# Kernel optimization log

Measured on AMD Instinct MI355X. Metric: run time of the kernel, lower is better.

Reference implementation:

```python
import jax, jax.numpy as jnp
import numpy as np

B, N, M, D = 8, 512, 64, 128
H = 64  # mlp_hidden_dim


def setup_inputs() -> dict:
    key = jax.random.key(0)
    ks = jax.random.split(key, 10)
    op_emb = jax.random.normal(ks[0], (B, N, D), dtype=jnp.float32)
    machine_emb = jax.random.normal(ks[1], (B, M, D), dtype=jnp.float32)
    edge_emb = jax.random.normal(ks[2], (B, N, M, D), dtype=jnp.float32)
    action_mask = jax.random.randint(ks[3], (B, N, M), 0, 2) > 0
    s1 = 1.0 / np.sqrt(3 * D)
    s2 = 1.0 / np.sqrt(H)
    W1 = jax.random.uniform(ks[4], (3 * D, H), jnp.float32, -s1, s1)
    b1 = jax.random.uniform(ks[5], (H,), jnp.float32, -s1, s1)
    W2 = jax.random.uniform(ks[6], (H, H), jnp.float32, -s2, s2)
    b2 = jax.random.uniform(ks[7], (H,), jnp.float32, -s2, s2)
    W3 = jax.random.uniform(ks[8], (H, 1), jnp.float32, -s2, s2)
    b3 = jax.random.uniform(ks[9], (1,), jnp.float32, -s2, s2)
    return {"op_emb": op_emb, "machine_emb": machine_emb, "edge_emb": edge_emb,
            "action_mask": action_mask,
            "W1": W1, "b1": b1, "W2": W2, "b2": b2, "W3": W3, "b3": b3}


def reference(op_emb, machine_emb, edge_emb, action_mask, W1, b1, W2, b2, W3, b3):
    # Split first linear over the three concat chunks to avoid materializing
    # the (B,N,M,3D) concat tensor (same math as cat -> Linear).
    Wo, Wm, We = W1[:D], W1[D:2 * D], W1[2 * D:]
    h = (jnp.einsum('bnd,dh->bnh', op_emb, Wo)[:, :, None, :]
         + jnp.einsum('bmd,dh->bmh', machine_emb, Wm)[:, None, :, :]
         + jnp.einsum('bnmd,dh->bnmh', edge_emb, We) + b1)  # (B,N,M,H)
    h = jax.nn.relu(h)
    h = jax.nn.relu(h @ W2 + b2)
    scores = (h @ W3 + b3)[..., 0]  # (B,N,M)
    scores = jnp.where(action_mask, scores, -jnp.inf)
    return jax.nn.log_softmax(scores.reshape(B, N * M), axis=-1)
```

## Files before the change

### kernel.cpp

```cpp
#include <hip/hip_runtime.h>
#include <math.h>

#define Bb 8
#define Nn 512
#define Mm 64
#define Dd 128
#define Hh 64
#define Gg 8
#define NEG_BIG (-1.0e30f)

#define SEGF 260
#define BUFF (8 * SEGF)

typedef __bf16 bf16x8 __attribute__((ext_vector_type(8)));
typedef float  f32x4  __attribute__((ext_vector_type(4)));

#define WS_WEB   0u
#define WS_W2B   16384u
#define WS_CWSF  24576u
#define WS_AOP   155648u
#define WS_SCORE 1204224u
#define WS_PART  2252800u

#define GLOAD_LDS(gp, lp) __builtin_amdgcn_global_load_lds( \
    (const __attribute__((address_space(1))) void*)(gp),    \
    (__attribute__((address_space(3))) void*)(lp), 16, 0, 0)

__global__ __launch_bounds__(256) void prep_kernel(
    const float* __restrict__ W1, const float* __restrict__ W2,
    const float* __restrict__ op_emb, const float* __restrict__ machine_emb,
    const float* __restrict__ b1, char* __restrict__ ws)
{
    if (blockIdx.x < 48) {
        __bf16* WeB = (__bf16*)(ws + WS_WEB);
        __bf16* W2B = (__bf16*)(ws + WS_W2B);
        int idx = blockIdx.x * 256 + threadIdx.x;
        if (idx < 8192) {
            int fid = idx >> 9, rem = idx & 511;
            int lane = rem >> 3, j = rem & 7;
            int t = fid >> 2, ks = fid & 3;
            int q = lane >> 4, ln = lane & 15;
            int d = ks * 32 + q * 8 + j;
            int h = t * 16 + ln;
            WeB[idx] = (__bf16)W1[(size_t)(2 * Dd + d) * Hh + h];
        } else {
            int i2 = idx - 8192;
            int fid = i2 >> 9, rem = i2 & 511;
            int lane = rem >> 3, j = rem & 7;
            int t = fid >> 1, ks = fid & 1;
            int q = lane >> 4, ln = lane & 15;
            int k = ks * 32 + q * 8 + j;
            int h = t * 16 + ln;
            W2B[i2] = (__bf16)W2[(size_t)k * Hh + h];
        }
        return;
    }
    float* CwsF = (float*)(ws + WS_CWSF);
    float* Aop  = (float*)(ws + WS_AOP);
    const int bid = (blockIdx.x - 48) * 4 + (threadIdx.x >> 6);
    const int h = threadIdx.x & 63;
    if (bid < Bb * Mm) {
        const float* mg = machine_emb + (size_t)bid * Dd;
        const float* Wm = W1 + (size_t)Dd * Hh;
        float acc = b1[h];
#pragma unroll 8
        for (int d = 0; d < Dd; ++d) acc = fmaf(mg[d], Wm[d * Hh + h], acc);
        int b = bid >> 6, m = bid & 63;
        int wq = m >> 4, q = (m >> 2) & 3, r = m & 3;
        int t = h >> 4, ln = h & 15;
        CwsF[((((b * 4 + wq) * 4 + t) * 64) + (q * 16 + ln)) * 4 + r] = acc;
    } else {
        const int bn = bid - Bb * Mm;
        const float* og = op_emb + (size_t)bn * Dd;
        float acc = 0.f;
#pragma unroll 8
        for (int d = 0; d < Dd; ++d) acc = fmaf(og[d], W1[d * Hh + h], acc);
        Aop[(size_t)bn * Hh + h] = acc;
    }
}

__global__ __launch_bounds__(256, 2) void main_kernel(
    const float* __restrict__ edge_emb, const int* __restrict__ mask,
    const float* __restrict__ b2, const float* __restrict__ W3,
    const float* __restrict__ b3, char* __restrict__ ws)
{
    __shared__ float  sEdge[4 * 2 * BUFF];
    __shared__ float  sAop[Gg * Hh];
    __shared__ int    sMask[Gg * Mm];
    __shared__ __bf16 sH1[Mm * 72];
    __shared__ float  sRed[8];

    float* scores = (float*)(ws + WS_SCORE);
    float* part   = (float*)(ws + WS_PART);

    const int tid  = threadIdx.x;
    const int lane = tid & 63;
    const int w    = tid >> 6;
    const int q    = lane >> 4;
    const int ln   = lane & 15;
    const int bn0  = blockIdx.x * Gg;
    const int b    = bn0 >> 9;
    const int wu   = __builtin_amdgcn_readfirstlane(w);

    const float* ebase = edge_emb + (size_t)bn0 * (Mm * Dd) + w * 2048 + lane * 4;

    {
        float* d0 = &sEdge[(wu * 2 + 0) * BUFF];
        float* d1 = &sEdge[(wu * 2 + 1) * BUFF];
#pragma unroll
        for (int s = 0; s < 8; ++s) GLOAD_LDS(ebase + s * 256, d0 + s * SEGF);
#pragma unroll
        for (int s = 0; s < 8; ++s) GLOAD_LDS(ebase + 8192 + s * 256, d1 + s * SEGF);
    }

    if (tid < 128) {
        ((f32x4*)sAop)[tid] = ((const f32x4*)(ws + WS_AOP))[(size_t)bn0 * 16 + tid];
        ((int4*)sMask)[tid] = ((const int4*)mask)[(size_t)bn0 * 16 + tid];
    }

    bf16x8 weF[16], w2F[8];
    f32x4  cv[4];
    {
        const bf16x8* WeB = (const bf16x8*)(ws + WS_WEB);
        const bf16x8* W2B = (const bf16x8*)(ws + WS_W2B);
#pragma unroll
        for (int f = 0; f < 16; ++f) weF[f] = WeB[f * 64 + lane];
#pragma unroll
        for (int f = 0; f < 8; ++f)  w2F[f] = W2B[f * 64 + lane];
        const f32x4* CwsF = (const f32x4*)(ws + WS_CWSF) + (size_t)b * 1024;
#pragma unroll
        for (int t = 0; t < 4; ++t)  cv[t] = CwsF[(w * 4 + t) * 64 + lane];
    }

    float b2v[4], w3v[4];
#pragma unroll
    for (int t = 0; t < 4; ++t) { b2v[t] = b2[t * 16 + ln]; w3v[t] = W3[t * 16 + ln]; }
    const float bias3 = b3[0];

    const int rdoff = (ln >> 1) * SEGF + (ln & 1) * 128 + q * 8;

    float m_loc = NEG_BIG, l_loc = 0.f;

    __syncthreads();

#pragma unroll
    for (int g = 0; g < Gg; ++g) {
        const int buf = g & 1;
        const float* ldsrd = &sEdge[(wu * 2 + buf) * BUFF];

        if (g == Gg - 1) __builtin_amdgcn_s_waitcnt(0x0F70);
        else             __builtin_amdgcn_s_waitcnt(0x0F78);

        f32x4 lo[4], hi[4];
#pragma unroll
        for (int ks = 0; ks < 4; ++ks) {
            lo[ks] = *(const f32x4*)&ldsrd[rdoff + ks * 32];
            hi[ks] = *(const f32x4*)&ldsrd[rdoff + ks * 32 + 4];
        }
        bf16x8 af[4];
#pragma unroll
        for (int ks = 0; ks < 4; ++ks) {
            bf16x8 a;
            a[0] = (__bf16)lo[ks][0]; a[1] = (__bf16)lo[ks][1];
            a[2] = (__bf16)lo[ks][2]; a[3] = (__bf16)lo[ks][3];
            a[4] = (__bf16)hi[ks][0]; a[5] = (__bf16)hi[ks][1];
            a[6] = (__bf16)hi[ks][2]; a[7] = (__bf16)hi[ks][3];
            af[ks] = a;
        }

        if (g + 2 < Gg) {
            float* dst = &sEdge[(wu * 2 + buf) * BUFF];
            const float* src = ebase + (size_t)(g + 2) * 8192;
#pragma unroll
            for (int s = 0; s < 8; ++s) GLOAD_LDS(src + s * 256, dst + s * SEGF);
        }

        f32x4 acc[4];
#pragma unroll
        for (int t = 0; t < 4; ++t) {
            float av = sAop[g * Hh + t * 16 + ln];
            acc[t][0] = cv[t][0] + av; acc[t][1] = cv[t][1] + av;
            acc[t][2] = cv[t][2] + av; acc[t][3] = cv[t][3] + av;
        }

#pragma unroll
        for (int t = 0; t < 4; ++t)
#pragma unroll
            for (int ks = 0; ks < 4; ++ks)
                acc[t] = __builtin_amdgcn_mfma_f32_16x16x32_bf16(af[ks], weF[t * 4 + ks], acc[t], 0, 0, 0);

#pragma unroll
        for (int t = 0; t < 4; ++t)
#pragma unroll
            for (int r = 0; r < 4; ++r)
                sH1[(w * 16 + q * 4 + r) * 72 + t * 16 + ln] =
                    (__bf16)fmaxf(acc[t][r], 0.f);

        bf16x8 a2[2];
#pragma unroll
        for (int ks = 0; ks < 2; ++ks)
            a2[ks] = *(const bf16x8*)&sH1[(w * 16 + ln) * 72 + ks * 32 + q * 8];
        f32x4 c2[4];
#pragma unroll
        for (int t = 0; t < 4; ++t) c2[t] = (f32x4){0.f, 0.f, 0.f, 0.f};
#pragma unroll
        for (int t = 0; t < 4; ++t)
#pragma unroll
            for (int ks = 0; ks < 2; ++ks)
                c2[t] = __builtin_amdgcn_mfma_f32_16x16x32_bf16(a2[ks], w2F[t * 2 + ks], c2[t], 0, 0, 0);

        float p[4] = {0.f, 0.f, 0.f, 0.f};
#pragma unroll
        for (int t = 0; t < 4; ++t)
#pragma unroll
            for (int r = 0; r < 4; ++r)
                p[r] += fmaxf(c2[t][r] + b2v[t], 0.f) * w3v[t];
#pragma unroll
        for (int r = 0; r < 4; ++r) {
            p[r] += __shfl_xor(p[r], 1, 64);
            p[r] += __shfl_xor(p[r], 2, 64);
            p[r] += __shfl_xor(p[r], 4, 64);
            p[r] += __shfl_xor(p[r], 8, 64);
        }
        const int m0 = w * 16 + q * 4;
        const int* mrow = &sMask[g * Mm + m0];
        float vv[4];
#pragma unroll
        for (int r = 0; r < 4; ++r) {
            float v = p[r] + bias3;
            vv[r] = mrow[r] ? v : NEG_BIG;
            if (mrow[r]) {
                float mn = fmaxf(m_loc, v);
                l_loc = l_loc * expf(m_loc - mn) + expf(v - mn);
                m_loc = mn;
            }
        }
        if (ln == 0) {
            float4 o; o.x = vv[0]; o.y = vv[1]; o.z = vv[2]; o.w = vv[3];
            *(float4*)&scores[(size_t)(bn0 + g) * Mm + m0] = o;
        }
    }

#pragma unroll
    for (int off = 16; off <= 32; off <<= 1) {
        float mo = __shfl_xor(m_loc, off, 64);
        float lo2 = __shfl_xor(l_loc, off, 64);
        float mn = fmaxf(m_loc, mo);
        l_loc = l_loc * expf(m_loc - mn) + lo2 * expf(mo - mn);
        m_loc = mn;
    }
    if (lane == 0) { sRed[w * 2] = m_loc; sRed[w * 2 + 1] = l_loc; }
    __syncthreads();
    if (tid == 0) {
        float gm = sRed[0], gl = sRed[1];
#pragma unroll
        for (int k = 1; k < 4; ++k) {
            float mo = sRed[k * 2], lo2 = sRed[k * 2 + 1];
            float mn = fmaxf(gm, mo);
            gl = gl * expf(gm - mn) + lo2 * expf(mo - mn);
            gm = mn;
        }
        float2 o; o.x = gm; o.y = gl;
        *(float2*)&part[blockIdx.x * 2] = o;
    }
}

__global__ __launch_bounds__(256) void lsm_apply_kernel(
    const char* __restrict__ ws, float* __restrict__ out)
{
    const float4* s4 = (const float4*)(ws + WS_SCORE);
    const float* part = (const float*)(ws + WS_PART);
    __shared__ float sCC;
    const int tid = threadIdx.x;
    const int b = blockIdx.x >> 5;
    if (tid < 64) {
        float2 p = *(const float2*)&part[(b * 64 + tid) * 2];
        float gm = p.x;
#pragma unroll
        for (int off = 1; off < 64; off <<= 1) gm = fmaxf(gm, __shfl_xor(gm, off, 64));
        float l = p.y * expf(p.x - gm);
#pragma unroll
        for (int off = 1; off < 64; off <<= 1) l += __shfl_xor(l, off, 64);
        if (tid == 0) sCC = gm + logf(l);
    }
    __syncthreads();
    const float c = sCC;
    const int i = blockIdx.x * 256 + tid;
    float4 v = s4[i];
    v.x -= c; v.y -= c; v.z -= c; v.w -= c;
    ((float4*)out)[i] = v;
}

extern "C" void kernel_launch(void* const* d_in, const int* in_sizes, int n_in,
                              void* d_out, int out_size, void* d_ws, size_t ws_size,
                              hipStream_t stream)
{
    const float* op_emb      = (const float*)d_in[0];
    const float* machine_emb = (const float*)d_in[1];
    const float* edge_emb    = (const float*)d_in[2];
    const int*   mask        = (const int*)  d_in[3];
    const float* W1 = (const float*)d_in[4];
    const float* b1 = (const float*)d_in[5];
    const float* W2 = (const float*)d_in[6];
    const float* b2 = (const float*)d_in[7];
    const float* W3 = (const float*)d_in[8];
    const float* b3 = (const float*)d_in[9];
    char* ws = (char*)d_ws;

    prep_kernel<<<48 + 1152, 256, 0, stream>>>(W1, W2, op_emb, machine_emb, b1, ws);
    main_kernel<<<(Bb * Nn) / Gg, 256, 0, stream>>>(edge_emb, mask, b2, W3, b3, ws);
    lsm_apply_kernel<<<256, 256, 0, stream>>>(ws, (float*)d_out);
}
```

Measured before the change: 228.1 us.

## Fuse machine and op projections into main kernel, shrink prep kernel

Moves the per-batch machine-embedding projection and the per-row op-embedding projection out of the prep kernel and into the main kernel. The machine term is computed with bf16 MFMA from a tile staged through the existing LDS double buffer, and the op term with scalar FMAs per block. Prep now only converts weights to bf16 fragments, so its grid drops from 1200 blocks to 80. This removes the workspace round trip for the precomputed terms, at the cost of redundant per-block work: every block recomputes the machine projection for its batch and reads W1 rows from global memory with scalar loads. It also adds register pressure from an extra 16 weight fragments.

Measured after the change: 228.8 us. No clear change (+0.3%).

```diff
diff --git a/kernel.cpp b/kernel.cpp
--- a/kernel.cpp
+++ b/kernel.cpp
@@ -16,71 +16,47 @@
 typedef float  f32x4  __attribute__((ext_vector_type(4)));
 
 #define WS_WEB   0u
-#define WS_W2B   16384u
-#define WS_CWSF  24576u
-#define WS_AOP   155648u
-#define WS_SCORE 1204224u
-#define WS_PART  2252800u
+#define WS_WMB   16384u
+#define WS_W2B   32768u
+#define WS_SCORE 49152u
+#define WS_PART  1097728u
 
 #define GLOAD_LDS(gp, lp) __builtin_amdgcn_global_load_lds( \
     (const __attribute__((address_space(1))) void*)(gp),    \
     (__attribute__((address_space(3))) void*)(lp), 16, 0, 0)
 
 __global__ __launch_bounds__(256) void prep_kernel(
-    const float* __restrict__ W1, const float* __restrict__ W2,
-    const float* __restrict__ op_emb, const float* __restrict__ machine_emb,
-    const float* __restrict__ b1, char* __restrict__ ws)
+    const float* __restrict__ W1, const float* __restrict__ W2, char* __restrict__ ws)
 {
-    if (blockIdx.x < 48) {
-        __bf16* WeB = (__bf16*)(ws + WS_WEB);
-        __bf16* W2B = (__bf16*)(ws + WS_W2B);
-        int idx = blockIdx.x * 256 + threadIdx.x;
-        if (idx < 8192) {
-            int fid = idx >> 9, rem = idx & 511;
-            int lane = rem >> 3, j = rem & 7;
-            int t = fid >> 2, ks = fid & 3;
-            int q = lane >> 4, ln = lane & 15;
-            int d = ks * 32 + q * 8 + j;
-            int h = t * 16 + ln;
-            WeB[idx] = (__bf16)W1[(size_t)(2 * Dd + d) * Hh + h];
-        } else {
-            int i2 = idx - 8192;
-            int fid = i2 >> 9, rem = i2 & 511;
-            int lane = rem >> 3, j = rem & 7;
-            int t = fid >> 1, ks = fid & 1;
-            int q = lane >> 4, ln = lane & 15;
-            int k = ks * 32 + q * 8 + j;
-            int h = t * 16 + ln;
-            W2B[i2] = (__bf16)W2[(size_t)k * Hh + h];
-        }
-        return;
-    }
-    float* CwsF = (float*)(ws + WS_CWSF);
-    float* Aop  = (float*)(ws + WS_AOP);
-    const int bid = (blockIdx.x - 48) * 4 + (threadIdx.x >> 6);
-    const int h = threadIdx.x & 63;
-    if (bid < Bb * Mm) {
-        const float* mg = machine_emb + (size_t)bid * Dd;
-        const float* Wm = W1 + (size_t)Dd * Hh;
-        float acc = b1[h];
-#pragma unroll 8
-        for (int d = 0; d < Dd; ++d) acc = fmaf(mg[d], Wm[d * Hh + h], acc);
-        int b = bid >> 6, m = bid & 63;
-        int wq = m >> 4, q = (m >> 2) & 3, r = m & 3;
-        int t = h >> 4, ln = h & 15;
-        CwsF[((((b * 4 + wq) * 4 + t) * 64) + (q * 16 + ln)) * 4 + r] = acc;
-    } else {
-        const int bn = bid - Bb * Mm;
-        const float* og = op_emb + (size_t)bn * Dd;
-        float acc = 0.f;
-#pragma unroll 8
-        for (int d = 0; d < Dd; ++d) acc = fmaf(og[d], W1[d * Hh + h], acc);
-        Aop[(size_t)bn * Hh + h] = acc;
+    int idx = blockIdx.x * 256 + threadIdx.x;
+    if (idx < 16384) {
+        int e = idx & 8191;
+        int fid = e >> 9, rem = e & 511;
+        int lane = rem >> 3, j = rem & 7;
+        int t = fid >> 2, ks = fid & 3;
+        int q = lane >> 4, ln = lane & 15;
+        int d = ks * 32 + q * 8 + j;
+        int h = t * 16 + ln;
+        if (idx < 8192)
+            ((__bf16*)(ws + WS_WEB))[e] = (__bf16)W1[(size_t)(2 * Dd + d) * Hh + h];
+        else
+            ((__bf16*)(ws + WS_WMB))[e] = (__bf16)W1[(size_t)(Dd + d) * Hh + h];
+    } else if (idx < 20480) {
+        int e = idx - 16384;
+        int fid = e >> 9, rem = e & 511;
+        int lane = rem >> 3, j = rem & 7;
+        int t = fid >> 1, ks = fid & 1;
+        int q = lane >> 4, ln = lane & 15;
+        int k = ks * 32 + q * 8 + j;
+        int h = t * 16 + ln;
+        ((__bf16*)(ws + WS_W2B))[e] = (__bf16)W2[(size_t)k * Hh + h];
     }
 }
 
 __global__ __launch_bounds__(256, 2) void main_kernel(
-    const float* __restrict__ edge_emb, const int* __restrict__ mask,
+    const float* __restrict__ edge_emb, const float* __restrict__ machine_emb,
+    const float* __restrict__ op_emb, const float* __restrict__ W1,
+    const float* __restrict__ b1, const int* __restrict__ mask,
     const float* __restrict__ b2, const float* __restrict__ W3,
     const float* __restrict__ b3, char* __restrict__ ws)
 {
@@ -102,42 +78,92 @@
     const int b    = bn0 >> 9;
     const int wu   = __builtin_amdgcn_readfirstlane(w);
 
+    bf16x8 weF[16], w2F[8], wmF[16];
+    {
+        const bf16x8* WeB = (const bf16x8*)(ws + WS_WEB);
+        const bf16x8* WmB = (const bf16x8*)(ws + WS_WMB);
+        const bf16x8* W2B = (const bf16x8*)(ws + WS_W2B);
+#pragma unroll
+        for (int f = 0; f < 16; ++f) weF[f] = WeB[f * 64 + lane];
+#pragma unroll
+        for (int f = 0; f < 16; ++f) wmF[f] = WmB[f * 64 + lane];
+#pragma unroll
+        for (int f = 0; f < 8; ++f)  w2F[f] = W2B[f * 64 + lane];
+    }
+
     const float* ebase = edge_emb + (size_t)bn0 * (Mm * Dd) + w * 2048 + lane * 4;
+    const float* mbase = machine_emb + (size_t)b * (Mm * Dd) + w * 2048 + lane * 4;
 
     {
         float* d0 = &sEdge[(wu * 2 + 0) * BUFF];
         float* d1 = &sEdge[(wu * 2 + 1) * BUFF];
 #pragma unroll
-        for (int s = 0; s < 8; ++s) GLOAD_LDS(ebase + s * 256, d0 + s * SEGF);
-#pragma unroll
-        for (int s = 0; s < 8; ++s) GLOAD_LDS(ebase + 8192 + s * 256, d1 + s * SEGF);
-    }
-
-    if (tid < 128) {
-        ((f32x4*)sAop)[tid] = ((const f32x4*)(ws + WS_AOP))[(size_t)bn0 * 16 + tid];
+        for (int s = 0; s < 8; ++s) GLOAD_LDS(mbase + s * 256, d0 + s * SEGF);
+#pragma unroll
+        for (int s = 0; s < 8; ++s) GLOAD_LDS(ebase + s * 256, d1 + s * SEGF);
+    }
+
+    {
+        const int an = tid >> 5;
+        const int ah = (tid * 2) & 63;
+        const float* orow = op_emb + (size_t)(bn0 + an) * Dd;
+        float a0 = 0.f, a1 = 0.f;
+#pragma unroll 8
+        for (int d = 0; d < Dd; ++d) {
+            float o = orow[d];
+            a0 = fmaf(o, W1[d * Hh + ah], a0);
+            a1 = fmaf(o, W1[d * Hh + ah + 1], a1);
+        }
+        sAop[an * 64 + ah] = a0;
+        sAop[an * 64 + ah + 1] = a1;
+    }
+    if (tid < 128)
         ((int4*)sMask)[tid] = ((const int4*)mask)[(size_t)bn0 * 16 + tid];
-    }
-
-    bf16x8 weF[16], w2F[8];
-    f32x4  cv[4];
+
+    float b2v[4], w3v[4], b1v[4];
+#pragma unroll
+    for (int t = 0; t < 4; ++t) {
+        b2v[t] = b2[t * 16 + ln]; w3v[t] = W3[t * 16 + ln]; b1v[t] = b1[t * 16 + ln];
+    }
+    const float bias3 = b3[0];
+
+    const int rdoff = (ln >> 1) * SEGF + (ln & 1) * 128 + q * 8;
+
+    f32x4 cv[4];
     {
-        const bf16x8* WeB = (const bf16x8*)(ws + WS_WEB);
-        const bf16x8* W2B = (const bf16x8*)(ws + WS_W2B);
-#pragma unroll
-        for (int f = 0; f < 16; ++f) weF[f] = WeB[f * 64 + lane];
-#pragma unroll
-        for (int f = 0; f < 8; ++f)  w2F[f] = W2B[f * 64 + lane];
-        const f32x4* CwsF = (const f32x4*)(ws + WS_CWSF) + (size_t)b * 1024;
-#pragma unroll
-        for (int t = 0; t < 4; ++t)  cv[t] = CwsF[(w * 4 + t) * 64 + lane];
-    }
-
-    float b2v[4], w3v[4];
-#pragma unroll
-    for (int t = 0; t < 4; ++t) { b2v[t] = b2[t * 16 + ln]; w3v[t] = W3[t * 16 + ln]; }
-    const float bias3 = b3[0];
-
-    const int rdoff = (ln >> 1) * SEGF + (ln & 1) * 128 + q * 8;
+        __builtin_amdgcn_s_waitcnt(0x0F78);
+        const float* ldsrd = &sEdge[(wu * 2 + 0) * BUFF];
+        f32x4 lo[4], hi[4];
+#pragma unroll
+        for (int ks = 0; ks < 4; ++ks) {
+            lo[ks] = *(const f32x4*)&ldsrd[rdoff + ks * 32];
+            hi[ks] = *(const f32x4*)&ldsrd[rdoff + ks * 32 + 4];
+        }
+        bf16x8 am[4];
+#pragma unroll
+        for (int ks = 0; ks < 4; ++ks) {
+            bf16x8 a;
+            a[0] = (__bf16)lo[ks][0]; a[1] = (__bf16)lo[ks][1];
+            a[2] = (__bf16)lo[ks][2]; a[3] = (__bf16)lo[ks][3];
+            a[4] = (__bf16)hi[ks][0]; a[5] = (__bf16)hi[ks][1];
+            a[6] = (__bf16)hi[ks][2]; a[7] = (__bf16)hi[ks][3];
+            am[ks] = a;
+        }
+        {
+            float* dst = &sEdge[(wu * 2 + 0) * BUFF];
+            const float* src = ebase + 8192;
+#pragma unroll
+            for (int s = 0; s < 8; ++s) GLOAD_LDS(src + s * 256, dst + s * SEGF);
+        }
+#pragma unroll
+        for (int t = 0; t < 4; ++t)
+            cv[t] = (f32x4){b1v[t], b1v[t], b1v[t], b1v[t]};
+#pragma unroll
+        for (int t = 0; t < 4; ++t)
+#pragma unroll
+            for (int ks = 0; ks < 4; ++ks)
+                cv[t] = __builtin_amdgcn_mfma_f32_16x16x32_bf16(am[ks], wmF[t * 4 + ks], cv[t], 0, 0, 0);
+    }
 
     float m_loc = NEG_BIG, l_loc = 0.f;
 
@@ -145,7 +171,7 @@
 
 #pragma unroll
     for (int g = 0; g < Gg; ++g) {
-        const int buf = g & 1;
+        const int buf = (g + 1) & 1;
         const float* ldsrd = &sEdge[(wu * 2 + buf) * BUFF];
 
         if (g == Gg - 1) __builtin_amdgcn_s_waitcnt(0x0F70);
@@ -177,24 +203,21 @@
 
         f32x4 acc[4];
 #pragma unroll
+        for (int t = 0; t < 4; ++t) acc[t] = (f32x4){0.f, 0.f, 0.f, 0.f};
+#pragma unroll
+        for (int t = 0; t < 4; ++t)
+#pragma unroll
+            for (int ks = 0; ks < 4; ++ks)
+                acc[t] = __builtin_amdgcn_mfma_f32_16x16x32_bf16(af[ks], weF[t * 4 + ks], acc[t], 0, 0, 0);
+
+#pragma unroll
         for (int t = 0; t < 4; ++t) {
             float av = sAop[g * Hh + t * 16 + ln];
-            acc[t][0] = cv[t][0] + av; acc[t][1] = cv[t][1] + av;
-            acc[t][2] = cv[t][2] + av; acc[t][3] = cv[t][3] + av;
-        }
-
-#pragma unroll
-        for (int t = 0; t < 4; ++t)
-#pragma unroll
-            for (int ks = 0; ks < 4; ++ks)
-                acc[t] = __builtin_amdgcn_mfma_f32_16x16x32_bf16(af[ks], weF[t * 4 + ks], acc[t], 0, 0, 0);
-
-#pragma unroll
-        for (int t = 0; t < 4; ++t)
 #pragma unroll
             for (int r = 0; r < 4; ++r)
                 sH1[(w * 16 + q * 4 + r) * 72 + t * 16 + ln] =
-                    (__bf16)fmaxf(acc[t][r], 0.f);
+                    (__bf16)fmaxf(acc[t][r] + av + cv[t][r], 0.f);
+        }
 
         bf16x8 a2[2];
 #pragma unroll
@@ -307,7 +330,8 @@
     const float* b3 = (const float*)d_in[9];
     char* ws = (char*)d_ws;
 
-    prep_kernel<<<48 + 1152, 256, 0, stream>>>(W1, W2, op_emb, machine_emb, b1, ws);
-    main_kernel<<<(Bb * Nn) / Gg, 256, 0, stream>>>(edge_emb, mask, b2, W3, b3, ws);
+    prep_kernel<<<80, 256, 0, stream>>>(W1, W2, ws);
+    main_kernel<<<(Bb * Nn) / Gg, 256, 0, stream>>>(edge_emb, machine_emb, op_emb,
+                                                    W1, b1, mask, b2, W3, b3, ws);
     lsm_apply_kernel<<<256, 256, 0, stream>>>(ws, (float*)d_out);
 }
```
